# Kernel optimization log

Measured on AMD Instinct MI355X. Metric: run time of the kernel, lower is better.

The kernel has to match this reference:

```python
import jax, jax.numpy as jnp
import numpy as np

B, D, N = 64, 768, 196          # batch, channels (input_dim=output_dim=linear_out), spatial tokens of x
LIN, CIN, COUT = 1536, 196, 196  # linear_in, conv_dim_in, conv_dim_out
T, DM, DD = 32, 384, 96          # num_tokens, d_model=linear_out//2, bottleneck=768//8
EPS = 1e-5
ALPHA, BETA = 0.3, 0.05


def _linear(h, w, b):
    return h @ w.T + b


def _ln(h, g, b):  # layernorm over last axis
    mu = h.mean(-1, keepdims=True)
    var = ((h - mu) ** 2).mean(-1, keepdims=True)
    return (h - mu) * jax.lax.rsqrt(var + EPS) * g + b


def _bn(h, g, b):  # BatchNorm2d training-mode stats over (batch, spatial), h: [B,C,N]
    mu = h.mean(axis=(0, 2), keepdims=True)
    var = ((h - mu) ** 2).mean(axis=(0, 2), keepdims=True)
    return (h - mu) * jax.lax.rsqrt(var + EPS) * g[None, :, None] + b[None, :, None]


def setup_inputs() -> dict:
    key = jax.random.key(0)
    ks = iter(jax.random.split(key, 32))
    def nrm(shape, s=0.02):
        return jax.random.normal(next(ks), shape, jnp.float32) * s
    return dict(
        x=jax.random.normal(next(ks), (B, D, N, 1), jnp.float32),
        vis_token=jax.random.normal(next(ks), (B, LIN, CIN, 1), jnp.float32),
        conv_w=nrm((COUT, CIN)), conv_b=nrm((COUT,)),
        fc_w=nrm((D, LIN)), fc_b=nrm((D,)),
        a1_w=nrm((D, D)), a1_b=nrm((D,)),
        v1_w=nrm((D, D)), v1_b=nrm((D,)),
        btl_w=nrm((DM, D)), btl_b=nrm((DM,)),
        v2_w=nrm((DM, D)), v2_b=nrm((DM,)),
        a2_w=nrm((DM, D)), a2_b=nrm((DM,)),
        vs_w=nrm((1, DM)), vs_b=nrm((1,)),
        vc_w=nrm((D, DM)), vc_b=nrm((D,)),
        my_tokens=nrm((T, D)),
        gate_av=jnp.float32(0.5), gate=jnp.float32(0.5),
        down_w=nrm((DD, D)), up_w=nrm((D, DD)),
        bn1_g=jnp.ones((DD,), jnp.float32), bn1_b=jnp.zeros((DD,), jnp.float32),
        bn2_g=jnp.ones((D,), jnp.float32), bn2_b=jnp.zeros((D,), jnp.float32),
        lnb_g=jnp.ones((D,), jnp.float32), lnb_b=jnp.zeros((D,), jnp.float32),
        lnp_g=jnp.ones((D,), jnp.float32), lnp_b=jnp.zeros((D,), jnp.float32),
    )


def reference(x, vis_token, conv_w, conv_b, fc_w, fc_b, a1_w, a1_b, v1_w, v1_b,
              btl_w, btl_b, v2_w, v2_b, a2_w, a2_b, vs_w, vs_b, vc_w, vc_b,
              my_tokens, gate_av, gate, down_w, up_w,
              bn1_g, bn1_b, bn2_g, bn2_b, lnb_g, lnb_b, lnp_g, lnp_b):
    # conv_adapter on vis_token.transpose(2,1): 1x1 conv over conv_dim_in channels
    vtc = jnp.einsum('blc,oc->bol', vis_token[..., 0], conv_w) + conv_b[None, :, None]  # [B,COUT,LIN]
    vtf = _linear(vtc, fc_w, fc_b)          # [B,COUT,D]
    vt3 = vtf.transpose(0, 2, 1)            # [B,D,M]  (vis_token.squeeze(-1))

    # token <- vis attention
    att_v2tk = jax.nn.softmax(jnp.einsum('td,bdm->btm', my_tokens, vt3), axis=-1)
    rep = my_tokens[None] + jnp.einsum('btm,bdm->btd', att_v2tk, vt3)  # [B,T,D]

    # x <- token attention
    xT = x[..., 0].transpose(0, 2, 1)       # [B,N,D]
    att_tk2x = jax.nn.softmax(jnp.einsum('bnd,btd->bnt', xT, rep), axis=-1)
    xT = xT + gate_av * jnp.einsum('bnt,btd->bnd', att_tk2x, rep)

    # channel / spatial gating
    audio = vt3.mean(axis=2)                                  # [B,D]
    aq1 = jax.nn.relu(_linear(audio, a1_w, a1_b))[:, None, :]  # [B,1,D]
    vq1 = jax.nn.relu(_linear(xT, v1_w, v1_b))                 # [B,N,D]
    avq = jax.nn.relu(_linear((aq1 * vq1).mean(1), btl_w, btl_b))  # [B,DM]
    ch_att = jax.nn.sigmoid(_linear(avq, vc_w, vc_b))[:, None, :]  # [B,1,D]
    c_feat = xT * (ch_att + 1.0)
    c_q = jax.nn.relu(_linear(c_feat, v2_w, v2_b))             # [B,N,DM]
    aq2 = jax.nn.relu(_linear(audio, a2_w, a2_b))[:, None, :]  # [B,1,DM]
    s_tmp = _linear(c_q * aq2, vs_w, vs_b)                     # [B,N,1]
    s_sig = jax.nn.sigmoid(s_tmp)                              # [B,N,1]
    sp_att = jax.nn.softmax(jnp.tanh(s_tmp).transpose(0, 2, 1), axis=-1)  # [B,1,N]

    xT = xT * (ALPHA * ch_att + BETA * s_sig + (1.0 - ALPHA))

    # ln_before + bottleneck conv down/up with BN
    xT = _ln(xT, lnb_g, lnb_b)
    x3 = xT.transpose(0, 2, 1)                                # [B,D,N]
    z = jax.nn.relu(_bn(jnp.einsum('bdn,ed->ben', x3, down_w), bn1_g, bn1_b))
    out = _bn(jnp.einsum('ben,de->bdn', z, up_w), bn2_g, bn2_b)
    out = _ln(out.transpose(0, 2, 1), lnp_g, lnp_b).transpose(0, 2, 1)[..., None]
    out = gate * out                                          # [B,D,N,1]
    return out, sp_att
```

## Files before the change

### kernel.cpp

```cpp
#include <hip/hip_runtime.h>
#include <math.h>

#define BB 64
#define DD0 768
#define NN 196
#define LIN 1536
#define CIN 196
#define COUT 196
#define TT 32
#define DM 384
#define DDB 96
#define EPS 1e-5f
#define MFLAT (BB * NN)
#define NCONV (BB * LIN)

#define OFF_A     0LL
#define OFF_B     9633792LL
#define OFF_XT    19267584LL
#define OFF_REP   28901376LL
#define OFF_Y1    30474240LL
#define OFF_WCONV 31678464LL
#define OFF_WFC   31698064LL
#define OFF_WV1   32287888LL
#define OFF_WV2   32582800LL
#define OFF_SM    32730256LL
#define OFF_AUDIO (OFF_SM)
#define OFF_AQ1   (OFF_SM+49152)
#define OFF_MVQ   (OFF_SM+98304)
#define OFF_AVQ   (OFF_SM+147456)
#define OFF_CHATT (OFF_SM+172032)
#define OFF_AQ2   (OFF_SM+221184)
#define OFF_SSIG  (OFF_SM+245760)
#define OFF_STATS (OFF_SM+258304)
#define OFF_PBUF  (OFF_SM+262144)
#define OFF_WDOWN (OFF_SM+491520)
#define OFF_WUP   (OFF_SM+528384)
#define OFF_STMP  (OFF_SM+565248)

typedef __attribute__((ext_vector_type(8))) short short8;
typedef __attribute__((ext_vector_type(4))) float f32x4;

__device__ __forceinline__ unsigned short f2bf(float f) {
    union { float f; unsigned u; } v; v.f = f;
    unsigned r = v.u + 0x7fffu + ((v.u >> 16) & 1u);
    return (unsigned short)(r >> 16);
}
__device__ __forceinline__ short8 cvt8(const float4 a, const float4 b) {
    short8 r;
    r[0] = (short)f2bf(a.x); r[1] = (short)f2bf(a.y); r[2] = (short)f2bf(a.z); r[3] = (short)f2bf(a.w);
    r[4] = (short)f2bf(b.x); r[5] = (short)f2bf(b.y); r[6] = (short)f2bf(b.z); r[7] = (short)f2bf(b.w);
    return r;
}
__device__ __forceinline__ short8 lds_frag(const unsigned short* p) {
    short4 lo = *(const short4*)p;
    short4 hi = *(const short4*)(p + 4);
    short8 r;
    r[0] = lo.x; r[1] = lo.y; r[2] = lo.z; r[3] = lo.w;
    r[4] = hi.x; r[5] = hi.y; r[6] = hi.z; r[7] = hi.w;
    return r;
}

__device__ __forceinline__ float warp_sum(float v) {
    for (int o = 32; o; o >>= 1) v += __shfl_down(v, o, 64);
    return v;
}
__device__ __forceinline__ float wave_allsum(float v) {
    for (int o = 1; o < 64; o <<= 1) v += __shfl_xor(v, o, 64);
    return v;
}
__device__ __forceinline__ float wave_allmax(float v) {
    for (int o = 1; o < 64; o <<= 1) v = fmaxf(v, __shfl_xor(v, o, 64));
    return v;
}
__device__ __forceinline__ float warp_max(float v) {
    for (int o = 32; o; o >>= 1) v = fmaxf(v, __shfl_down(v, o, 64));
    return v;
}
__device__ __forceinline__ float block_sum256(float v, float* sb) {
    v = warp_sum(v);
    __syncthreads();
    if ((threadIdx.x & 63) == 0) sb[threadIdx.x >> 6] = v;
    __syncthreads();
    return sb[0] + sb[1] + sb[2] + sb[3];
}
__device__ __forceinline__ float block_max256(float v, float* sb) {
    v = warp_max(v);
    __syncthreads();
    if ((threadIdx.x & 63) == 0) sb[threadIdx.x >> 6] = v;
    __syncthreads();
    return fmaxf(fmaxf(sb[0], sb[1]), fmaxf(sb[2], sb[3]));
}

template<int MODE, bool ABF, bool BBF, bool KSC, int EPI, bool NG>
__global__ __launch_bounds__(256)
void gemm_mfma(const void* __restrict__ Ap, int lda,
               const void* __restrict__ Bp, int ldb,
               const float* __restrict__ bias, const float* __restrict__ ksc,
               void* __restrict__ Cp, int M, int N, int K, int Ka)
{
    __shared__ unsigned short Asm[128][72];
    __shared__ unsigned short Bsm[128][72];
    const int tid = threadIdx.x;
    const int m0 = blockIdx.y * 128, n0 = blockIdx.x * 128;
    const int w = tid >> 6, lane = tid & 63;
    const int wr = w >> 1, wc = w & 1;

    f32x4 acc[4][4];
    #pragma unroll
    for (int i = 0; i < 4; i++)
        #pragma unroll
        for (int j = 0; j < 4; j++) acc[i][j] = (f32x4){0.f, 0.f, 0.f, 0.f};

    const int nkt = (K + 63) >> 6;
    for (int kt = 0; kt < nkt; kt++) {
        const int k0 = kt << 6;
        if (ABF) {
            #pragma unroll
            for (int q = 0; q < 4; q++) {
                const int row = q * 32 + (tid >> 3);
                const int ce = (tid & 7) * 8;
                const int gm = m0 + row;
                const bool rok = (MODE == 1) ? (gm < M) : true;
                uint4 u = make_uint4(0u, 0u, 0u, 0u);
                if (rok && (k0 + ce) < Ka)
                    u = *(const uint4*)((const unsigned short*)Ap + (long long)gm * lda + k0 + ce);
                *(uint4*)&Asm[row][ce] = u;
            }
        } else {
            #pragma unroll
            for (int q = 0; q < 8; q++) {
                const int row = q * 16 + (tid >> 4);
                const int ce = (tid & 15) * 4;
                const int gm = m0 + row;
                const bool rok = (MODE == 1) ? (gm < M) : true;
                float4 v = make_float4(0.f, 0.f, 0.f, 0.f);
                const bool kok = (k0 + ce) < K;
                if (rok && kok)
                    v = *(const float4*)((const float*)Ap + (long long)gm * lda + k0 + ce);
                if (KSC && kok) {
                    const float* kc = ksc + (gm / 196) * 768 + k0 + ce;
                    v.x *= kc[0] + 1.f; v.y *= kc[1] + 1.f;
                    v.z *= kc[2] + 1.f; v.w *= kc[3] + 1.f;
                }
                ushort4 o; o.x = f2bf(v.x); o.y = f2bf(v.y); o.z = f2bf(v.z); o.w = f2bf(v.w);
                *(ushort4*)&Asm[row][ce] = o;
            }
        }
        if (BBF) {
            #pragma unroll
            for (int q = 0; q < 4; q++) {
                const int row = q * 32 + (tid >> 3);
                const int ce = (tid & 7) * 8;
                const int gn = n0 + row;
                const bool nok = NG ? (gn < N) : true;
                uint4 u = make_uint4(0u, 0u, 0u, 0u);
                if (nok && (k0 + ce) < K)
                    u = *(const uint4*)((const unsigned short*)Bp + (long long)gn * ldb + k0 + ce);
                *(uint4*)&Bsm[row][ce] = u;
            }
        } else {
            #pragma unroll
            for (int q = 0; q < 8; q++) {
                const int row = q * 16 + (tid >> 4);
                const int ce = (tid & 15) * 4;
                const int gn = n0 + row;
                const bool nok = NG ? (gn < N) : true;
                float4 v = make_float4(0.f, 0.f, 0.f, 0.f);
                if (nok && (k0 + ce) < K)
                    v = *(const float4*)((const float*)Bp + (long long)gn * ldb + k0 + ce);
                ushort4 o; o.x = f2bf(v.x); o.y = f2bf(v.y); o.z = f2bf(v.z); o.w = f2bf(v.w);
                *(ushort4*)&Bsm[row][ce] = o;
            }
        }
        __syncthreads();
        #pragma unroll
        for (int kk = 0; kk < 2; kk++) {
            short8 af[4], bfr[4];
            const int koff = kk * 32 + (lane >> 4) * 8;
            #pragma unroll
            for (int i = 0; i < 4; i++)
                af[i] = *(const short8*)&Asm[wr * 64 + i * 16 + (lane & 15)][koff];
            #pragma unroll
            for (int j = 0; j < 4; j++)
                bfr[j] = *(const short8*)&Bsm[wc * 64 + j * 16 + (lane & 15)][koff];
            #pragma unroll
            for (int i = 0; i < 4; i++)
                #pragma unroll
                for (int j = 0; j < 4; j++)
                    acc[i][j] = __builtin_amdgcn_mfma_f32_16x16x32_bf16(af[i], bfr[j], acc[i][j], 0, 0, 0);
        }
        __syncthreads();
    }
    const int cmb = wr * 64 + ((lane >> 4) << 2);
    const int cnb = wc * 64 + (lane & 15);
    #pragma unroll
    for (int i = 0; i < 4; i++) {
        #pragma unroll
        for (int j = 0; j < 4; j++) {
            const int gn = n0 + cnb + j * 16;
            if (NG && gn >= N) continue;
            #pragma unroll
            for (int rr = 0; rr < 4; rr++) {
                const int gm = m0 + cmb + i * 16 + rr;
                float v = acc[i][j][rr];
                if (MODE == 0) {
                    if (bias) v += bias[gn];
                    if (EPI == 1) v = fmaxf(v, 0.f);
                    ((float*)Cp)[(long long)gm * N + gn] = v;
                } else {
                    if (gm < M) {
                        v += bias[gm];
                        const int b = gn / LIN, l = gn - b * LIN;
                        ((unsigned short*)Cp)[((long long)b * COUT + gm) * LIN + l] = f2bf(v);
                    }
                }
            }
        }
    }
}

__global__ void cvt_f2bf(const float* __restrict__ in, unsigned short* __restrict__ out, int n)
{
    int i = (blockIdx.x * 256 + threadIdx.x) * 4;
    if (i + 4 <= n) {
        float4 v = *(const float4*)(in + i);
        ushort4 o; o.x = f2bf(v.x); o.y = f2bf(v.y); o.z = f2bf(v.z); o.w = f2bf(v.w);
        *(ushort4*)(out + i) = o;
    }
}
__global__ void cvt_f2bf_pad(const float* __restrict__ in, unsigned short* __restrict__ out,
                             int rows, int cols, int ldo)
{
    int i = blockIdx.x * 256 + threadIdx.x;
    if (i < rows * ldo) {
        int r = i / ldo, c = i - r * ldo;
        out[i] = (c < cols) ? f2bf(in[r * cols + c]) : (unsigned short)0;
    }
}

template<int ACT>
__global__ __launch_bounds__(256)
void wave_gemv(const float* __restrict__ A, int lda,
               const float* __restrict__ B, int ldb,
               const float* __restrict__ bias,
               float* __restrict__ C, int N, int K)
{
    const int w = threadIdx.x >> 6, lane = threadIdx.x & 63;
    const long long o = (long long)blockIdx.x * 4 + w;
    const int m = (int)(o / N), n = (int)(o - (long long)m * N);
    const float* ar = A + (long long)m * lda;
    const float* br = B + (long long)n * ldb;
    float s = 0.f;
    for (int k = lane; k < K; k += 64) s += ar[k] * br[k];
    s = wave_allsum(s);
    if (lane == 0) {
        float v = s + bias[n];
        if (ACT == 1) v = fmaxf(v, 0.f);
        if (ACT == 2) v = 1.f / (1.f + expf(-v));
        C[o] = v;
    }
}

__global__ void transpose_kernel(const float* __restrict__ in, float* __restrict__ out,
                                 int D, int N)
{
    __shared__ float tile[32][33];
    int b = blockIdx.z;
    int d0 = blockIdx.y * 32, n0 = blockIdx.x * 32;
    int tx = threadIdx.x, ty = threadIdx.y;
    for (int i = 0; i < 32; i += 8) {
        int d = d0 + ty + i, n = n0 + tx;
        if (d < D && n < N) tile[ty + i][tx] = in[((long long)b * D + d) * N + n];
    }
    __syncthreads();
    for (int i = 0; i < 32; i += 8) {
        int n = n0 + ty + i, d = d0 + tx;
        if (n < N && d < D) out[((long long)b * N + n) * D + d] = tile[tx][ty + i];
    }
}

__global__ void audio_kernel(const float* __restrict__ vtf, float* __restrict__ audio)
{
    int b = blockIdx.y, d = blockIdx.x * 256 + threadIdx.x;
    float s = 0.f;
    for (int m = 0; m < COUT; m++) s += vtf[((long long)b * COUT + m) * DD0 + d];
    audio[b * DD0 + d] = s * (1.f / (float)COUT);
}

__global__ __launch_bounds__(256)
void att1_scores(const float* __restrict__ vtf, const float* __restrict__ mt,
                 unsigned short* __restrict__ pbuf)
{
    __shared__ float sc[TT][208];
    const int b = blockIdx.x;
    const int tid = threadIdx.x, w = tid >> 6, lane = tid & 63;
    const int l15 = lane & 15, kg = (lane >> 4) << 3;
    const float* vb = vtf + (long long)b * COUT * DD0;

    f32x4 acc[4][2];
    #pragma unroll
    for (int q = 0; q < 4; q++) { acc[q][0] = (f32x4){0.f,0.f,0.f,0.f}; acc[q][1] = (f32x4){0.f,0.f,0.f,0.f}; }

    for (int kt = 0; kt < DD0; kt += 32) {
        const float* a0p = mt + (long long)l15 * DD0 + kt + kg;
        const float* a1p = a0p + 16 * DD0;
        short8 a0 = cvt8(*(const float4*)a0p, *(const float4*)(a0p + 4));
        short8 a1 = cvt8(*(const float4*)a1p, *(const float4*)(a1p + 4));
        #pragma unroll
        for (int q = 0; q < 4; q++) {
            const int mtile = w + q * 4;
            const int gm = mtile * 16 + l15;
            short8 bf = {0,0,0,0,0,0,0,0};
            if (gm < COUT) {
                const float* bp = vb + (long long)gm * DD0 + kt + kg;
                bf = cvt8(*(const float4*)bp, *(const float4*)(bp + 4));
            }
            acc[q][0] = __builtin_amdgcn_mfma_f32_16x16x32_bf16(a0, bf, acc[q][0], 0, 0, 0);
            acc[q][1] = __builtin_amdgcn_mfma_f32_16x16x32_bf16(a1, bf, acc[q][1], 0, 0, 0);
        }
    }
    #pragma unroll
    for (int q = 0; q < 4; q++) {
        const int mtile = w + q * 4;
        if (mtile < 13) {
            #pragma unroll
            for (int j = 0; j < 2; j++)
                #pragma unroll
                for (int r = 0; r < 4; r++)
                    sc[j * 16 + ((lane >> 4) << 2) + r][mtile * 16 + l15] = acc[q][j][r];
        }
    }
    __syncthreads();
    for (int tr = 0; tr < 8; tr++) {
        const int t = w * 8 + tr;
        float v = -1e30f;
        for (int m = lane; m < COUT; m += 64) v = fmaxf(v, sc[t][m]);
        v = wave_allmax(v);
        float s = 0.f;
        for (int m = lane; m < COUT; m += 64) { float e = __expf(sc[t][m] - v); sc[t][m] = e; s += e; }
        s = wave_allsum(s);
        const float inv = 1.f / s;
        unsigned short* pr = pbuf + ((long long)b * TT + t) * 224;
        for (int m = lane; m < 224; m += 64) pr[m] = (m < COUT) ? f2bf(sc[t][m] * inv) : (unsigned short)0;
    }
}

__global__ __launch_bounds__(256)
void att1_pv(const float* __restrict__ vtf, const unsigned short* __restrict__ pbuf,
             const float* __restrict__ mt, float* __restrict__ rep)
{
    __shared__ unsigned short vT[128][36];
    const int b = blockIdx.y, d0 = blockIdx.x * 128;
    const int tid = threadIdx.x, w = tid >> 6, lane = tid & 63;
    const int l15 = lane & 15, kg = (lane >> 4) << 3;
    const float* vb = vtf + (long long)b * COUT * DD0;

    f32x4 acc[2][2];
    acc[0][0] = (f32x4){0.f,0.f,0.f,0.f}; acc[0][1] = (f32x4){0.f,0.f,0.f,0.f};
    acc[1][0] = (f32x4){0.f,0.f,0.f,0.f}; acc[1][1] = (f32x4){0.f,0.f,0.f,0.f};

    for (int kc = 0; kc < 7; kc++) {
        for (int i = tid; i < 32 * 128; i += 256) {
            const int m = i >> 7, dd = i & 127;
            const int gm = kc * 32 + m;
            const float v = (gm < COUT) ? vb[(long long)gm * DD0 + d0 + dd] : 0.f;
            vT[dd][m] = f2bf(v);
        }
        const short8 p0 = *(const short8*)(pbuf + ((long long)b * TT + l15) * 224 + kc * 32 + kg);
        const short8 p1 = *(const short8*)(pbuf + ((long long)b * TT + 16 + l15) * 224 + kc * 32 + kg);
        __syncthreads();
        #pragma unroll
        for (int jl = 0; jl < 2; jl++) {
            const short8 bf = lds_frag(&vT[(w * 2 + jl) * 16 + l15][kg]);
            acc[0][jl] = __builtin_amdgcn_mfma_f32_16x16x32_bf16(p0, bf, acc[0][jl], 0, 0, 0);
            acc[1][jl] = __builtin_amdgcn_mfma_f32_16x16x32_bf16(p1, bf, acc[1][jl], 0, 0, 0);
        }
        __syncthreads();
    }
    #pragma unroll
    for (int j = 0; j < 2; j++) {
        #pragma unroll
        for (int jl = 0; jl < 2; jl++) {
            const int t = j * 16 + ((lane >> 4) << 2);
            const int gd = d0 + (w * 2 + jl) * 16 + l15;
            #pragma unroll
            for (int r = 0; r < 4; r++)
                rep[((long long)b * TT + t + r) * DD0 + gd] = mt[(long long)(t + r) * DD0 + gd] + acc[j][jl][r];
        }
    }
}

__global__ __launch_bounds__(256)
void att2_mfma(const float* __restrict__ rep, const float* __restrict__ gav,
               float* __restrict__ xT)
{
    __shared__ unsigned short repT[DD0][36];
    __shared__ unsigned short Pl[64][36];
    const int b = blockIdx.y, m0 = blockIdx.x * 64;
    const int tid = threadIdx.x, w = tid >> 6, lane = tid & 63;
    const int l15 = lane & 15, kg = (lane >> 4) << 3;
    const float* repb = rep + (long long)b * TT * DD0;

    for (int i = tid; i < TT * DD0; i += 256) {
        const int t = i / DD0, d = i - t * DD0;
        repT[d][t] = f2bf(repb[i]);
    }
    __syncthreads();

    f32x4 acc0 = (f32x4){0.f,0.f,0.f,0.f}, acc1 = (f32x4){0.f,0.f,0.f,0.f};
    const int arow = m0 + w * 16 + l15;
    const bool rok = arow < NN;
    const float* xrow = xT + ((long long)b * NN + arow) * DD0;
    for (int kt = 0; kt < DD0; kt += 32) {
        short8 af = {0,0,0,0,0,0,0,0};
        if (rok) af = cvt8(*(const float4*)(xrow + kt + kg), *(const float4*)(xrow + kt + kg + 4));
        const float* r0 = repb + (long long)l15 * DD0 + kt + kg;
        const float* r1 = r0 + 16 * DD0;
        const short8 b0 = cvt8(*(const float4*)r0, *(const float4*)(r0 + 4));
        const short8 b1 = cvt8(*(const float4*)r1, *(const float4*)(r1 + 4));
        acc0 = __builtin_amdgcn_mfma_f32_16x16x32_bf16(af, b0, acc0, 0, 0, 0);
        acc1 = __builtin_amdgcn_mfma_f32_16x16x32_bf16(af, b1, acc1, 0, 0, 0);
    }
    #pragma unroll
    for (int r = 0; r < 4; r++) {
        float m = fmaxf(acc0[r], acc1[r]);
        m = fmaxf(m, __shfl_xor(m, 1, 64));
        m = fmaxf(m, __shfl_xor(m, 2, 64));
        m = fmaxf(m, __shfl_xor(m, 4, 64));
        m = fmaxf(m, __shfl_xor(m, 8, 64));
        const float e0 = __expf(acc0[r] - m), e1 = __expf(acc1[r] - m);
        float s = e0 + e1;
        s += __shfl_xor(s, 1, 64); s += __shfl_xor(s, 2, 64);
        s += __shfl_xor(s, 4, 64); s += __shfl_xor(s, 8, 64);
        const float inv = 1.f / s;
        const int prow = w * 16 + ((lane >> 4) << 2) + r;
        Pl[prow][l15] = f2bf(e0 * inv);
        Pl[prow][l15 + 16] = f2bf(e1 * inv);
    }
    __syncthreads();
    const short8 pa = lds_frag(&Pl[w * 16 + l15][kg]);
    const float ga = gav[0];
    const int gmb = m0 + w * 16 + ((lane >> 4) << 2);
    for (int jd = 0; jd < 48; jd++) {
        const short8 bf = lds_frag(&repT[jd * 16 + l15][kg]);
        f32x4 av = (f32x4){0.f,0.f,0.f,0.f};
        av = __builtin_amdgcn_mfma_f32_16x16x32_bf16(pa, bf, av, 0, 0, 0);
        const int gd = jd * 16 + l15;
        #pragma unroll
        for (int r = 0; r < 4; r++) {
            if (gmb + r < NN) {
                const long long idx = ((long long)b * NN + gmb + r) * DD0 + gd;
                xT[idx] += ga * av[r];
            }
        }
    }
}

__global__ void mvq_kernel(const float* __restrict__ vq1, const float* __restrict__ aq1,
                           float* __restrict__ mvq)
{
    int b = blockIdx.y, d = blockIdx.x * 256 + threadIdx.x;
    float s = 0.f;
    for (int n = 0; n < NN; n++) s += vq1[((long long)b * NN + n) * DD0 + d];
    mvq[b * DD0 + d] = aq1[b * DD0 + d] * s * (1.f / (float)NN);
}

__global__ __launch_bounds__(256)
void stmp_dot(const float* __restrict__ cq, const float* __restrict__ aq2,
              const float* __restrict__ vsw, const float* __restrict__ vsb,
              float* __restrict__ stb, float* __restrict__ ssig)
{
    const int b = blockIdx.y, tid = threadIdx.x, w = tid >> 6, lane = tid & 63;
    __shared__ float wv[DM];
    for (int i = tid; i < DM; i += 256) wv[i] = aq2[b * DM + i] * vsw[i];
    __syncthreads();
    const int n = blockIdx.x * 4 + w;
    const float* cr = cq + ((long long)b * NN + n) * DM;
    float s = 0.f;
    for (int d = lane; d < DM; d += 64) s += cr[d] * wv[d];
    s = wave_allsum(s);
    if (lane == 0) {
        const float sv = s + vsb[0];
        stb[b * NN + n] = tanhf(sv);
        ssig[b * NN + n] = 1.f / (1.f + expf(-sv));
    }
}

__global__ __launch_bounds__(256)
void stmp_soft(const float* __restrict__ stb, float* __restrict__ spatt)
{
    const int b = blockIdx.x, tid = threadIdx.x;
    __shared__ float sb[4];
    float v = (tid < NN) ? stb[b * NN + tid] : -1e30f;
    float mx = block_max256(v, sb);
    __syncthreads();
    float e = (tid < NN) ? __expf(v - mx) : 0.f;
    float s = block_sum256(e, sb);
    if (tid < NN) spatt[b * NN + tid] = e / s;
}

__global__ __launch_bounds__(256)
void scale_ln_kernel(float* __restrict__ xT, const float* __restrict__ chatt,
                     const float* __restrict__ ssig, const float* __restrict__ g,
                     const float* __restrict__ bb)
{
    int b = blockIdx.y, n = blockIdx.x, tid = threadIdx.x;
    __shared__ float sb[4];
    float* xr = xT + ((long long)b * NN + n) * DD0;
    float ss = ssig[b * NN + n];
    float v[3];
    float lsum = 0.f;
    #pragma unroll
    for (int i = 0; i < 3; i++) {
        int d = tid + i * 256;
        float sc = 0.3f * chatt[b * DD0 + d] + 0.05f * ss + 0.7f;
        v[i] = xr[d] * sc;
        lsum += v[i];
    }
    float mean = block_sum256(lsum, sb) * (1.f / (float)DD0);
    float lvar = 0.f;
    #pragma unroll
    for (int i = 0; i < 3; i++) { float dd = v[i] - mean; lvar += dd * dd; }
    float var = block_sum256(lvar, sb) * (1.f / (float)DD0);
    float inv = rsqrtf(var + EPS);
    #pragma unroll
    for (int i = 0; i < 3; i++) {
        int d = tid + i * 256;
        xr[d] = (v[i] - mean) * inv * g[d] + bb[d];
    }
}

__global__ void bn1stats_kernel(const float* __restrict__ y1, float* __restrict__ stats)
{
    int b = blockIdx.y, n0 = blockIdx.x * 49, tid = threadIdx.x;
    if (tid < DDB) {
        float s = 0.f, q = 0.f;
        for (int n = n0; n < n0 + 49; n++) {
            float v = y1[((long long)b * NN + n) * DDB + tid];
            s += v; q += v * v;
        }
        atomicAdd(&stats[tid], s);
        atomicAdd(&stats[DDB + tid], q);
    }
}

__global__ void bn1apply_kernel(float* __restrict__ y1, const float* __restrict__ stats,
                                const float* __restrict__ g, const float* __restrict__ bb)
{
    long long i = (long long)blockIdx.x * 256 + threadIdx.x;
    if (i >= (long long)BB * NN * DDB) return;
    int e = (int)(i % DDB);
    const float cnt = (float)(BB * NN);
    float mu = stats[e] / cnt;
    float var = stats[DDB + e] / cnt - mu * mu;
    float v = (y1[i] - mu) * rsqrtf(var + EPS) * g[e] + bb[e];
    y1[i] = fmaxf(v, 0.f);
}

__global__ void bn2stats_kernel(const float* __restrict__ y2, float* __restrict__ stats)
{
    int b = blockIdx.y, d = blockIdx.x * 256 + threadIdx.x;
    float s = 0.f, q = 0.f;
    for (int n = 0; n < NN; n++) {
        float v = y2[((long long)b * NN + n) * DD0 + d];
        s += v; q += v * v;
    }
    atomicAdd(&stats[d], s);
    atomicAdd(&stats[DD0 + d], q);
}

__global__ __launch_bounds__(256)
void final_kernel(const float* __restrict__ y2, const float* __restrict__ stats2,
                  const float* __restrict__ g2, const float* __restrict__ b2,
                  const float* __restrict__ lg, const float* __restrict__ lb,
                  const float* __restrict__ gate, float* __restrict__ out_tmp)
{
    int b = blockIdx.y, n = blockIdx.x, tid = threadIdx.x;
    __shared__ float sb[4];
    const float* yr = y2 + ((long long)b * NN + n) * DD0;
    const float cnt = (float)(BB * NN);
    float v[3];
    float lsum = 0.f;
    #pragma unroll
    for (int i = 0; i < 3; i++) {
        int d = tid + i * 256;
        float mu = stats2[d] / cnt;
        float var = stats2[DD0 + d] / cnt - mu * mu;
        v[i] = (yr[d] - mu) * rsqrtf(var + EPS) * g2[d] + b2[d];
        lsum += v[i];
    }
    float mean = block_sum256(lsum, sb) * (1.f / (float)DD0);
    float lvar = 0.f;
    #pragma unroll
    for (int i = 0; i < 3; i++) { float dd = v[i] - mean; lvar += dd * dd; }
    float var = block_sum256(lvar, sb) * (1.f / (float)DD0);
    float inv = rsqrtf(var + EPS);
    float gt = gate[0];
    float* orow = out_tmp + ((long long)b * NN + n) * DD0;
    #pragma unroll
    for (int i = 0; i < 3; i++) {
        int d = tid + i * 256;
        orow[d] = ((v[i] - mean) * inv * lg[d] + lb[d]) * gt;
    }
}

extern "C" void kernel_launch(void* const* d_in, const int* in_sizes, int n_in,
                              void* d_out, int out_size, void* d_ws, size_t ws_size,
                              hipStream_t stream)
{
    const float* x       = (const float*)d_in[0];
    const float* vis     = (const float*)d_in[1];
    const float* conv_w  = (const float*)d_in[2];
    const float* conv_b  = (const float*)d_in[3];
    const float* fc_w    = (const float*)d_in[4];
    const float* fc_b    = (const float*)d_in[5];
    const float* a1_w    = (const float*)d_in[6];
    const float* a1_b    = (const float*)d_in[7];
    const float* v1_w    = (const float*)d_in[8];
    const float* v1_b    = (const float*)d_in[9];
    const float* btl_w   = (const float*)d_in[10];
    const float* btl_b   = (const float*)d_in[11];
    const float* v2_w    = (const float*)d_in[12];
    const float* v2_b    = (const float*)d_in[13];
    const float* a2_w    = (const float*)d_in[14];
    const float* a2_b    = (const float*)d_in[15];
    const float* vs_w    = (const float*)d_in[16];
    const float* vs_b    = (const float*)d_in[17];
    const float* vc_w    = (const float*)d_in[18];
    const float* vc_b    = (const float*)d_in[19];
    const float* my_tok  = (const float*)d_in[20];
    const float* gate_av = (const float*)d_in[21];
    const float* gate    = (const float*)d_in[22];
    const float* down_w  = (const float*)d_in[23];
    const float* up_w    = (const float*)d_in[24];
    const float* bn1_g   = (const float*)d_in[25];
    const float* bn1_b   = (const float*)d_in[26];
    const float* bn2_g   = (const float*)d_in[27];
    const float* bn2_b   = (const float*)d_in[28];
    const float* lnb_g   = (const float*)d_in[29];
    const float* lnb_b   = (const float*)d_in[30];
    const float* lnp_g   = (const float*)d_in[31];
    const float* lnp_b   = (const float*)d_in[32];

    float* ws = (float*)d_ws;
    unsigned short* vtc_bf = (unsigned short*)(ws + OFF_A);
    float* vq1     = ws + OFF_A;
    float* cq      = ws + OFF_A;
    float* y2      = ws + OFF_A;
    float* vtf     = ws + OFF_B;
    float* out_tmp = ws + OFF_B;
    float* xT      = ws + OFF_XT;
    float* rep     = ws + OFF_REP;
    float* y1      = ws + OFF_Y1;
    unsigned short* wconv = (unsigned short*)(ws + OFF_WCONV);
    unsigned short* wfc   = (unsigned short*)(ws + OFF_WFC);
    unsigned short* wv1   = (unsigned short*)(ws + OFF_WV1);
    unsigned short* wv2   = (unsigned short*)(ws + OFF_WV2);
    unsigned short* wdown = (unsigned short*)(ws + OFF_WDOWN);
    unsigned short* wup   = (unsigned short*)(ws + OFF_WUP);
    float* audio   = ws + OFF_AUDIO;
    float* aq1b    = ws + OFF_AQ1;
    float* mvqb    = ws + OFF_MVQ;
    float* avqb    = ws + OFF_AVQ;
    float* chattb  = ws + OFF_CHATT;
    float* aq2b    = ws + OFF_AQ2;
    float* ssigb   = ws + OFF_SSIG;
    float* stats1  = ws + OFF_STATS;
    float* stats2  = ws + OFF_STATS + 2 * DDB;
    unsigned short* pbuf = (unsigned short*)(ws + OFF_PBUF);
    float* stbuf   = ws + OFF_STMP;

    float* out   = (float*)d_out;
    float* spatt = out + (long long)BB * DD0 * NN;

    hipMemsetAsync(stats1, 0, (2 * DDB + 2 * DD0) * sizeof(float), stream);

    cvt_f2bf<<<(DD0 * LIN / 4 + 255) / 256, 256, 0, stream>>>(fc_w, wfc, DD0 * LIN);
    cvt_f2bf<<<(DD0 * DD0 / 4 + 255) / 256, 256, 0, stream>>>(v1_w, wv1, DD0 * DD0);
    cvt_f2bf<<<(DM * DD0 / 4 + 255) / 256, 256, 0, stream>>>(v2_w, wv2, DM * DD0);
    cvt_f2bf<<<(DDB * DD0 / 4 + 255) / 256, 256, 0, stream>>>(down_w, wdown, DDB * DD0);
    cvt_f2bf<<<(DD0 * DDB / 4 + 255) / 256, 256, 0, stream>>>(up_w, wup, DD0 * DDB);
    cvt_f2bf_pad<<<(COUT * 200 + 255) / 256, 256, 0, stream>>>(conv_w, wconv, COUT, CIN, 200);

    transpose_kernel<<<dim3(7, 24, BB), dim3(32, 8), 0, stream>>>(x, xT, DD0, NN);
    gemm_mfma<1, true, false, false, 0, false><<<dim3(NCONV / 128, 2), 256, 0, stream>>>(
        wconv, 200, vis, CIN, conv_b, nullptr, vtc_bf, COUT, NCONV, CIN, 200);
    gemm_mfma<0, true, true, false, 0, false><<<dim3(DD0 / 128, MFLAT / 128), 256, 0, stream>>>(
        vtc_bf, LIN, wfc, LIN, fc_b, nullptr, vtf, MFLAT, DD0, LIN, LIN);
    audio_kernel<<<dim3(3, BB), 256, 0, stream>>>(vtf, audio);
    att1_scores<<<BB, 256, 0, stream>>>(vtf, my_tok, pbuf);
    att1_pv<<<dim3(6, BB), 256, 0, stream>>>(vtf, pbuf, my_tok, rep);
    att2_mfma<<<dim3(4, BB), 256, 0, stream>>>(rep, gate_av, xT);
    wave_gemv<1><<<BB * DD0 / 4, 256, 0, stream>>>(audio, DD0, a1_w, DD0, a1_b, aq1b, DD0, DD0);
    gemm_mfma<0, false, true, false, 1, false><<<dim3(DD0 / 128, MFLAT / 128), 256, 0, stream>>>(
        xT, DD0, wv1, DD0, v1_b, nullptr, vq1, MFLAT, DD0, DD0, DD0);
    mvq_kernel<<<dim3(3, BB), 256, 0, stream>>>(vq1, aq1b, mvqb);
    wave_gemv<1><<<BB * DM / 4, 256, 0, stream>>>(mvqb, DD0, btl_w, DD0, btl_b, avqb, DM, DD0);
    wave_gemv<2><<<BB * DD0 / 4, 256, 0, stream>>>(avqb, DM, vc_w, DM, vc_b, chattb, DD0, DM);
    wave_gemv<1><<<BB * DM / 4, 256, 0, stream>>>(audio, DD0, a2_w, DD0, a2_b, aq2b, DM, DD0);
    gemm_mfma<0, false, true, true, 1, false><<<dim3(DM / 128, MFLAT / 128), 256, 0, stream>>>(
        xT, DD0, wv2, DD0, v2_b, chattb, cq, MFLAT, DM, DD0, DD0);
    stmp_dot<<<dim3(49, BB), 256, 0, stream>>>(cq, aq2b, vs_w, vs_b, stbuf, ssigb);
    stmp_soft<<<BB, 256, 0, stream>>>(stbuf, spatt);
    scale_ln_kernel<<<dim3(NN, BB), 256, 0, stream>>>(xT, chattb, ssigb, lnb_g, lnb_b);
    gemm_mfma<0, false, true, false, 0, true><<<dim3(1, MFLAT / 128), 256, 0, stream>>>(
        xT, DD0, wdown, DD0, nullptr, nullptr, y1, MFLAT, DDB, DD0, DD0);
    bn1stats_kernel<<<dim3(4, BB), 128, 0, stream>>>(y1, stats1);
    bn1apply_kernel<<<(BB * NN * DDB + 255) / 256, 256, 0, stream>>>(y1, stats1, bn1_g, bn1_b);
    gemm_mfma<0, false, true, false, 0, false><<<dim3(DD0 / 128, MFLAT / 128), 256, 0, stream>>>(
        y1, DDB, wup, DDB, nullptr, nullptr, y2, MFLAT, DD0, DDB, DDB);
    bn2stats_kernel<<<dim3(3, BB), 256, 0, stream>>>(y2, stats2);
    final_kernel<<<dim3(NN, BB), 256, 0, stream>>>(y2, stats2, bn2_g, bn2_b,
                                                   lnp_g, lnp_b, gate, out_tmp);
    transpose_kernel<<<dim3(24, 7, BB), dim3(32, 8), 0, stream>>>(out_tmp, out, NN, DD0);
}
```

Before: 930.5 us.

## Add direct global-to-LDS bf16 GEMM with XCD swizzle for fc and v1 projections

Adds a new bf16 GEMM kernel that loads A and B tiles straight into LDS with global_load_lds, using an XOR-swizzled layout to avoid bank conflicts. It replaces the generic GEMM for the fc projection and the v1 projection; for v1 the fp32 xT is first converted to bf16 in a separate pass. Workgroup indices are remapped across XCDs in both GEMM kernels to improve L2 locality. The aim is to cut register staging and conversion overhead in the GEMM main loop. The cost is an extra conversion kernel and buffer, and the new kernel assumes M is a multiple of 128 and K a multiple of 64.

```diff
diff --git a/kernel.cpp b/kernel.cpp
--- a/kernel.cpp
+++ b/kernel.cpp
@@ -36,6 +36,7 @@
 #define OFF_WDOWN (OFF_SM+491520)
 #define OFF_WUP   (OFF_SM+528384)
 #define OFF_STMP  (OFF_SM+565248)
+#define OFF_XTBF  (OFF_SM+577792)
 
 typedef __attribute__((ext_vector_type(8))) short short8;
 typedef __attribute__((ext_vector_type(4))) float f32x4;
@@ -59,6 +60,16 @@
     r[4] = hi.x; r[5] = hi.y; r[6] = hi.z; r[7] = hi.w;
     return r;
 }
+__device__ __forceinline__ void gload16(const void* g, void* l) {
+    __builtin_amdgcn_global_load_lds(
+        (const __attribute__((address_space(1))) unsigned int*)g,
+        (__attribute__((address_space(3))) unsigned int*)l, 16, 0, 0);
+}
+__device__ __forceinline__ int xcd_swizzle(int orig, int nwg) {
+    const int q = nwg >> 3, r = nwg & 7;
+    const int x = orig & 7, lo = orig >> 3;
+    return (x < r ? x * (q + 1) : r * (q + 1) + (x - r) * q) + lo;
+}
 
 __device__ __forceinline__ float warp_sum(float v) {
     for (int o = 32; o; o >>= 1) v += __shfl_down(v, o, 64);
@@ -89,6 +100,87 @@
     if ((threadIdx.x & 63) == 0) sb[threadIdx.x >> 6] = v;
     __syncthreads();
     return fmaxf(fmaxf(sb[0], sb[1]), fmaxf(sb[2], sb[3]));
+}
+
+template<int EPI>
+__global__ __launch_bounds__(256)
+void gemm_gll(const unsigned short* __restrict__ Ap, int lda,
+              const unsigned short* __restrict__ Bp, int ldb,
+              const float* __restrict__ bias,
+              float* __restrict__ Cp, int N, int K)
+{
+    __shared__ unsigned short Asm[128 * 64];
+    __shared__ unsigned short Bsm[128 * 64];
+    const int nwg = gridDim.x * gridDim.y;
+    const int wg = xcd_swizzle(blockIdx.y * gridDim.x + blockIdx.x, nwg);
+    const int m0 = (wg / gridDim.x) * 128, n0 = (wg % gridDim.x) * 128;
+
+    const int tid = threadIdx.x, w = tid >> 6, lane = tid & 63;
+    const int wr = w >> 1, wc = w & 1;
+    const int soff = ((lane & 7) << 4) ^ ((lane >> 3) << 4);
+    const int arow = (lane >> 3);
+
+    f32x4 acc[4][4];
+    #pragma unroll
+    for (int i = 0; i < 4; i++)
+        #pragma unroll
+        for (int j = 0; j < 4; j++) acc[i][j] = (f32x4){0.f, 0.f, 0.f, 0.f};
+
+    for (int k0 = 0; k0 < K; k0 += 64) {
+        #pragma unroll
+        for (int q = 0; q < 4; q++) {
+            const int c = w * 4 + q;
+            const int row = c * 8 + arow;
+            const char* g = (const char*)Ap + (((long long)(m0 + row) * lda + k0) << 1) + soff;
+            gload16(g, (char*)Asm + c * 1024);
+        }
+        #pragma unroll
+        for (int q = 0; q < 4; q++) {
+            const int c = w * 4 + q;
+            const int row = c * 8 + arow;
+            const char* g = (const char*)Bp + (((long long)(n0 + row) * ldb + k0) << 1) + soff;
+            gload16(g, (char*)Bsm + c * 1024);
+        }
+        __syncthreads();
+        #pragma unroll
+        for (int kk = 0; kk < 2; kk++) {
+            const int kb = kk * 64 + ((lane >> 4) << 4);
+            const int swz = (lane & 7) << 4;
+            short8 af[4], bfr[4];
+            #pragma unroll
+            for (int i = 0; i < 4; i++) {
+                const int ra = wr * 64 + i * 16 + (lane & 15);
+                af[i] = *(const short8*)((const char*)Asm + ra * 128 + (kb ^ swz));
+            }
+            #pragma unroll
+            for (int j = 0; j < 4; j++) {
+                const int rb = wc * 64 + j * 16 + (lane & 15);
+                bfr[j] = *(const short8*)((const char*)Bsm + rb * 128 + (kb ^ swz));
+            }
+            #pragma unroll
+            for (int i = 0; i < 4; i++)
+                #pragma unroll
+                for (int j = 0; j < 4; j++)
+                    acc[i][j] = __builtin_amdgcn_mfma_f32_16x16x32_bf16(af[i], bfr[j], acc[i][j], 0, 0, 0);
+        }
+        __syncthreads();
+    }
+    const int cmb = wr * 64 + ((lane >> 4) << 2);
+    const int cnb = wc * 64 + (lane & 15);
+    #pragma unroll
+    for (int i = 0; i < 4; i++) {
+        #pragma unroll
+        for (int j = 0; j < 4; j++) {
+            const int gn = n0 + cnb + j * 16;
+            #pragma unroll
+            for (int rr = 0; rr < 4; rr++) {
+                const int gm = m0 + cmb + i * 16 + rr;
+                float v = acc[i][j][rr] + bias[gn];
+                if (EPI == 1) v = fmaxf(v, 0.f);
+                Cp[(long long)gm * N + gn] = v;
+            }
+        }
+    }
 }
 
 template<int MODE, bool ABF, bool BBF, bool KSC, int EPI, bool NG>
@@ -101,7 +193,9 @@
     __shared__ unsigned short Asm[128][72];
     __shared__ unsigned short Bsm[128][72];
     const int tid = threadIdx.x;
-    const int m0 = blockIdx.y * 128, n0 = blockIdx.x * 128;
+    const int nwg = gridDim.x * gridDim.y;
+    const int wg = xcd_swizzle(blockIdx.y * gridDim.x + blockIdx.x, nwg);
+    const int m0 = (wg / gridDim.x) * 128, n0 = (wg % gridDim.x) * 128;
     const int w = tid >> 6, lane = tid & 63;
     const int wr = w >> 1, wc = w & 1;
 
@@ -669,6 +763,7 @@
     float* stats2  = ws + OFF_STATS + 2 * DDB;
     unsigned short* pbuf = (unsigned short*)(ws + OFF_PBUF);
     float* stbuf   = ws + OFF_STMP;
+    unsigned short* xt_bf = (unsigned short*)(ws + OFF_XTBF);
 
     float* out   = (float*)d_out;
     float* spatt = out + (long long)BB * DD0 * NN;
@@ -685,15 +780,16 @@
     transpose_kernel<<<dim3(7, 24, BB), dim3(32, 8), 0, stream>>>(x, xT, DD0, NN);
     gemm_mfma<1, true, false, false, 0, false><<<dim3(NCONV / 128, 2), 256, 0, stream>>>(
         wconv, 200, vis, CIN, conv_b, nullptr, vtc_bf, COUT, NCONV, CIN, 200);
-    gemm_mfma<0, true, true, false, 0, false><<<dim3(DD0 / 128, MFLAT / 128), 256, 0, stream>>>(
-        vtc_bf, LIN, wfc, LIN, fc_b, nullptr, vtf, MFLAT, DD0, LIN, LIN);
+    gemm_gll<0><<<dim3(DD0 / 128, MFLAT / 128), 256, 0, stream>>>(
+        vtc_bf, LIN, wfc, LIN, fc_b, vtf, DD0, LIN);
     audio_kernel<<<dim3(3, BB), 256, 0, stream>>>(vtf, audio);
     att1_scores<<<BB, 256, 0, stream>>>(vtf, my_tok, pbuf);
     att1_pv<<<dim3(6, BB), 256, 0, stream>>>(vtf, pbuf, my_tok, rep);
     att2_mfma<<<dim3(4, BB), 256, 0, stream>>>(rep, gate_av, xT);
+    cvt_f2bf<<<(MFLAT * DD0 / 4 + 255) / 256, 256, 0, stream>>>(xT, xt_bf, MFLAT * DD0);
     wave_gemv<1><<<BB * DD0 / 4, 256, 0, stream>>>(audio, DD0, a1_w, DD0, a1_b, aq1b, DD0, DD0);
-    gemm_mfma<0, false, true, false, 1, false><<<dim3(DD0 / 128, MFLAT / 128), 256, 0, stream>>>(
-        xT, DD0, wv1, DD0, v1_b, nullptr, vq1, MFLAT, DD0, DD0, DD0);
+    gemm_gll<1><<<dim3(DD0 / 128, MFLAT / 128), 256, 0, stream>>>(
+        xt_bf, DD0, wv1, DD0, v1_b, vq1, DD0, DD0);
     mvq_kernel<<<dim3(3, BB), 256, 0, stream>>>(vq1, aq1b, mvqb);
     wave_gemv<1><<<BB * DM / 4, 256, 0, stream>>>(mvqb, DD0, btl_w, DD0, btl_b, avqb, DM, DD0);
     wave_gemv<2><<<BB * DD0 / 4, 256, 0, stream>>>(avqb, DM, vc_w, DM, vc_b, chattb, DD0, DM);
```

Result: faster. 860.3 us (-7.5%).
